# Kernel tuning notes

Measured on AMD Instinct MI355X. Metric: run time of the kernel, lower is better.

The kernel has to match this reference:

```python
import jax, jax.numpy as jnp
import numpy as np

N_NODES = 20000
N_EDGES = 640000
D = 128


def setup_inputs() -> dict:
    key = jax.random.key(0)
    ks = jax.random.split(key, 8)
    scale = 1.0 / np.sqrt(D)
    x = jax.random.normal(ks[0], (N_NODES, D), dtype=jnp.float32)
    edge_index = jax.random.randint(ks[1], (2, N_EDGES), 0, N_NODES, dtype=jnp.int64)
    W1_rel = jax.random.normal(ks[2], (D, D), dtype=jnp.float32) * scale
    b1_rel = jnp.zeros((D,), dtype=jnp.float32)
    W1_root = jax.random.normal(ks[3], (D, D), dtype=jnp.float32) * scale
    W2_rel = jax.random.normal(ks[4], (D, D), dtype=jnp.float32) * scale
    b2_rel = jnp.zeros((D,), dtype=jnp.float32)
    W2_root = jax.random.normal(ks[5], (D, D), dtype=jnp.float32) * scale
    return {"x": x, "edge_index": edge_index,
            "W1_rel": W1_rel, "b1_rel": b1_rel, "W1_root": W1_root,
            "W2_rel": W2_rel, "b2_rel": b2_rel, "W2_root": W2_root}


def _graph_conv(x, src, dst, W_rel, b_rel, W_root):
    # sum-aggregate neighbor features: gather from src, scatter-add to dst
    agg = jax.ops.segment_sum(x[src], dst, num_segments=N_NODES)  # [N, D]
    # PyG GraphConv: lin_rel(agg) (with bias) + lin_root(x) (no bias)
    return agg @ W_rel + b_rel + x @ W_root


def reference(x, edge_index, W1_rel, b1_rel, W1_root, W2_rel, b2_rel, W2_root):
    src, dst = edge_index[0], edge_index[1]  # messages flow src (j) -> dst (i)
    h = jax.nn.relu(_graph_conv(x, src, dst, W1_rel, b1_rel, W1_root))
    out = _graph_conv(h, src, dst, W2_rel, b2_rel, W2_root)  # final ReLU stripped
    return out
```

## Files before the change

kernel.cpp:

```cpp
#include <hip/hip_runtime.h>

#define N_NODES 20000
#define N_EDGES 640000
#define D 128
#define CAP 128

typedef __attribute__((ext_vector_type(8))) short bf16x8;
typedef __attribute__((ext_vector_type(4))) float f32x4;

__device__ __forceinline__ short f2bf(float f) {
    union { float f; unsigned u; } un; un.f = f;
    unsigned r = un.u + 0x7fff + ((un.u >> 16) & 1);
    return (short)(r >> 16);
}
__device__ __forceinline__ float bflo(unsigned u) { return __uint_as_float(u << 16); }
__device__ __forceinline__ float bfhi(unsigned u) { return __uint_as_float(u & 0xffff0000u); }

__global__ __launch_bounds__(256) void prep_kernel(
    const float* __restrict__ x,
    const int* __restrict__ src, const int* __restrict__ dst,
    const float* __restrict__ W1_rel, const float* __restrict__ W1_root,
    const float* __restrict__ W2_rel, const float* __restrict__ W2_root,
    int* __restrict__ cnt, unsigned short* __restrict__ buckets,
    short* __restrict__ xb, short* __restrict__ wpk1, short* __restrict__ wpk2)
{
    const int b = blockIdx.x;
    const int tid = threadIdx.x;
    if (b < 2500) {
        int e = b * 256 + tid;
        int d = dst[e];
        int s = src[e];
        int p = atomicAdd(&cnt[d], 1);
        if (p < CAP) buckets[(d << 7) + p] = (unsigned short)s;
    } else if (b < 5000) {
        int i = (b - 2500) * 256 + tid;
        float4 v = ((const float4*)x)[i];
        ushort4 o;
        o.x = (unsigned short)f2bf(v.x);
        o.y = (unsigned short)f2bf(v.y);
        o.z = (unsigned short)f2bf(v.z);
        o.w = (unsigned short)f2bf(v.w);
        ((ushort4*)xb)[i] = o;
    } else {
        int pb  = b - 5000;
        int job = pb >> 4;
        int idx = (pb & 15) * 256 + tid;
        const float* Wrel  = job ? W2_rel  : W1_rel;
        const float* Wroot = job ? W2_root : W1_root;
        short* Wpk = job ? wpk2 : wpk1;
        int lane = idx & 63;
        int ct   = (idx >> 6) & 7;
        int t    = idx >> 9;
        const float* W = (t < 4) ? Wrel : Wroot;
        int k0  = (t & 3) * 32 + (lane >> 4) * 8;
        int col = ct * 16 + (lane & 15);
        bf16x8 pk;
#pragma unroll
        for (int j = 0; j < 8; j++)
            pk[j] = f2bf(W[(size_t)(k0 + j) * D + col]);
        ((bf16x8*)Wpk)[idx] = pk;
    }
}

template <bool RELU, bool OUT_BF16>
__global__ __launch_bounds__(512) void layer_kernel(
    const short* __restrict__ xin,
    const int* __restrict__ cnt,
    const unsigned short* __restrict__ buckets,
    const short* __restrict__ Wpk,
    const float* __restrict__ brel,
    void* __restrict__ outp)
{
    __shared__ short sAgg[16][136];

    const int tid  = threadIdx.x;
    const int row0 = blockIdx.x * 16;

    {
        const int hw   = tid >> 5;
        const int lane = tid & 31;
        const int node = row0 + hw;
        int n = cnt[node];
        n = (n > CAP) ? CAP : n;
        uint2 idxpk = *(const uint2*)(buckets + (node << 7) + lane * 4);

        float4 acc = make_float4(0.f, 0.f, 0.f, 0.f);
        int i = 0;
        for (; i + 8 <= n; i += 8) {
            int baseLane = i >> 2;
            uint2 u[8];
#pragma unroll
            for (int q = 0; q < 8; q++) {
                unsigned word = __shfl((q & 2) ? idxpk.y : idxpk.x,
                                       baseLane + (q >> 2), 32);
                unsigned sidx = (q & 1) ? (word >> 16) : (word & 0xffffu);
                u[q] = *(const uint2*)(xin + (size_t)sidx * D + lane * 4);
            }
#pragma unroll
            for (int q = 0; q < 8; q++) {
                acc.x += bflo(u[q].x); acc.y += bfhi(u[q].x);
                acc.z += bflo(u[q].y); acc.w += bfhi(u[q].y);
            }
        }
        for (; i < n; i++) {
            unsigned word = __shfl((i & 2) ? idxpk.y : idxpk.x, i >> 2, 32);
            unsigned sidx = (i & 1) ? (word >> 16) : (word & 0xffffu);
            uint2 u0 = *(const uint2*)(xin + (size_t)sidx * D + lane * 4);
            acc.x += bflo(u0.x); acc.y += bfhi(u0.x);
            acc.z += bflo(u0.y); acc.w += bfhi(u0.y);
        }
        ushort4 o;
        o.x = (unsigned short)f2bf(acc.x);
        o.y = (unsigned short)f2bf(acc.y);
        o.z = (unsigned short)f2bf(acc.z);
        o.w = (unsigned short)f2bf(acc.w);
        *(ushort4*)&sAgg[hw][lane * 4] = o;
    }
    __syncthreads();

    const int wave = tid >> 6;
    const int lane = tid & 63;
    const int quad = lane >> 4;
    const int l16  = lane & 15;

    f32x4 acc = (f32x4){0.f, 0.f, 0.f, 0.f};
    const short* arow_x = xin + (size_t)(row0 + l16) * D + quad * 8;
    const bf16x8* wb = (const bf16x8*)Wpk + lane;

#pragma unroll
    for (int t = 0; t < 8; t++) {
        bf16x8 a;
        if (t < 4)
            a = *(const bf16x8*)&sAgg[l16][(t & 3) * 32 + quad * 8];
        else
            a = *(const bf16x8*)(arow_x + (t & 3) * 32);
        bf16x8 bfr = wb[(t * 8 + wave) * 64];
        acc = __builtin_amdgcn_mfma_f32_16x16x32_bf16(a, bfr, acc, 0, 0, 0);
    }

    const int col  = wave * 16 + l16;
    const int orow = row0 + quad * 4;
    const float bias = brel[col];
#pragma unroll
    for (int r = 0; r < 4; r++) {
        float v = acc[r] + bias;
        if (RELU) v = fmaxf(v, 0.f);
        if (OUT_BF16)
            ((short*)outp)[(size_t)(orow + r) * D + col] = f2bf(v);
        else
            ((float*)outp)[(size_t)(orow + r) * D + col] = v;
    }
}

extern "C" void kernel_launch(void* const* d_in, const int* in_sizes, int n_in,
                              void* d_out, int out_size, void* d_ws, size_t ws_size,
                              hipStream_t stream) {
    const float* x       = (const float*)d_in[0];
    const int*   ei      = (const int*)  d_in[1];
    const float* W1_rel  = (const float*)d_in[2];
    const float* b1_rel  = (const float*)d_in[3];
    const float* W1_root = (const float*)d_in[4];
    const float* W2_rel  = (const float*)d_in[5];
    const float* b2_rel  = (const float*)d_in[6];
    const float* W2_root = (const float*)d_in[7];
    float* out = (float*)d_out;

    char* p = (char*)d_ws;
    short* xb   = (short*)p;  p += (size_t)N_NODES * D * 2;
    short* hb   = (short*)p;  p += (size_t)N_NODES * D * 2;
    short* wpk1 = (short*)p;  p += 65536;
    short* wpk2 = (short*)p;  p += 65536;
    int*   cnt  = (int*)p;    p += (size_t)N_NODES * 4;
    unsigned short* buckets = (unsigned short*)p;

    const int* src = ei;
    const int* dst = ei + N_EDGES;

    const int layerblocks = N_NODES / 16;

    hipMemsetAsync(cnt, 0, (size_t)N_NODES * sizeof(int), stream);
    prep_kernel<<<5032, 256, 0, stream>>>(
        x, src, dst, W1_rel, W1_root, W2_rel, W2_root,
        cnt, buckets, xb, wpk1, wpk2);

    layer_kernel<true, true><<<layerblocks, 512, 0, stream>>>(
        xb, cnt, buckets, wpk1, b1_rel, (void*)hb);

    layer_kernel<false, false><<<layerblocks, 512, 0, stream>>>(
        hb, cnt, buckets, wpk2, b2_rel, (void*)out);
}
```

Baseline: 162.6 us.

## Replace global per-node atomic bucketing with two-pass binned CSR build

New measurement: 149.9 us. 1.08x faster.

```diff
diff --git a/kernel.cpp b/kernel.cpp
--- a/kernel.cpp
+++ b/kernel.cpp
@@ -4,6 +4,8 @@
 #define N_EDGES 640000
 #define D 128
 #define CAP 128
+#define NBINS 157
+#define BINCAP 4608
 
 typedef __attribute__((ext_vector_type(8))) short bf16x8;
 typedef __attribute__((ext_vector_type(4))) float f32x4;
@@ -21,19 +23,46 @@
     const int* __restrict__ src, const int* __restrict__ dst,
     const float* __restrict__ W1_rel, const float* __restrict__ W1_root,
     const float* __restrict__ W2_rel, const float* __restrict__ W2_root,
-    int* __restrict__ cnt, unsigned short* __restrict__ buckets,
+    int* __restrict__ binCursor, unsigned* __restrict__ binned,
     short* __restrict__ xb, short* __restrict__ wpk1, short* __restrict__ wpk2)
 {
     const int b = blockIdx.x;
     const int tid = threadIdx.x;
-    if (b < 2500) {
-        int e = b * 256 + tid;
-        int d = dst[e];
-        int s = src[e];
-        int p = atomicAdd(&cnt[d], 1);
-        if (p < CAP) buckets[(d << 7) + p] = (unsigned short)s;
-    } else if (b < 5000) {
-        int i = (b - 2500) * 256 + tid;
+    if (b < 256) {
+        __shared__ int hist[NBINS];
+        __shared__ int sBase[NBINS];
+        __shared__ int sOff[NBINS];
+        for (int i = tid; i < NBINS; i += 256) { hist[i] = 0; sOff[i] = 0; }
+        __syncthreads();
+        const int e0 = b * 2500;
+        int d[10], s[10];
+#pragma unroll
+        for (int k = 0; k < 10; k++) {
+            int idx = k * 256 + tid;
+            if (idx < 2500) {
+                d[k] = dst[e0 + idx];
+                s[k] = src[e0 + idx];
+                atomicAdd(&hist[d[k] >> 7], 1);
+            } else {
+                d[k] = -1;
+            }
+        }
+        __syncthreads();
+        for (int i = tid; i < NBINS; i += 256)
+            sBase[i] = atomicAdd(&binCursor[i], hist[i]);
+        __syncthreads();
+#pragma unroll
+        for (int k = 0; k < 10; k++) {
+            if (d[k] >= 0) {
+                int bin = d[k] >> 7;
+                int off = sBase[bin] + atomicAdd(&sOff[bin], 1);
+                if (off < BINCAP)
+                    binned[bin * BINCAP + off] =
+                        ((unsigned)(d[k] & 127) << 16) | (unsigned)s[k];
+            }
+        }
+    } else if (b < 2756) {
+        int i = (b - 256) * 256 + tid;
         float4 v = ((const float4*)x)[i];
         ushort4 o;
         o.x = (unsigned short)f2bf(v.x);
@@ -42,7 +71,7 @@
         o.w = (unsigned short)f2bf(v.w);
         ((ushort4*)xb)[i] = o;
     } else {
-        int pb  = b - 5000;
+        int pb  = b - 2756;
         int job = pb >> 4;
         int idx = (pb & 15) * 256 + tid;
         const float* Wrel  = job ? W2_rel  : W1_rel;
@@ -62,6 +91,30 @@
     }
 }
 
+__global__ __launch_bounds__(256) void binplace_kernel(
+    const unsigned* __restrict__ binned, const int* __restrict__ binCursor,
+    unsigned short* __restrict__ buckets, int* __restrict__ cnt)
+{
+    __shared__ int lcnt[128];
+    const int bin = blockIdx.x;
+    const int tid = threadIdx.x;
+    if (tid < 128) lcnt[tid] = 0;
+    __syncthreads();
+    int n = binCursor[bin];
+    if (n > BINCAP) n = BINCAP;
+    const unsigned* rec = binned + bin * BINCAP;
+    for (int i = tid; i < n; i += 256) {
+        unsigned u = rec[i];
+        int nl = (int)(u >> 16);
+        int slot = atomicAdd(&lcnt[nl], 1);
+        if (slot < CAP)
+            buckets[(((bin << 7) | nl) << 7) + slot] = (unsigned short)(u & 0xffffu);
+    }
+    __syncthreads();
+    int node = (bin << 7) + tid;
+    if (tid < 128 && node < N_NODES) cnt[node] = lcnt[tid];
+}
+
 template <bool RELU, bool OUT_BF16>
 __global__ __launch_bounds__(512) void layer_kernel(
     const short* __restrict__ xin,
@@ -172,16 +225,22 @@
     short* wpk2 = (short*)p;  p += 65536;
     int*   cnt  = (int*)p;    p += (size_t)N_NODES * 4;
     unsigned short* buckets = (unsigned short*)p;
+    p += (size_t)N_NODES * CAP * 2;
+    unsigned* binned = (unsigned*)p;
+    p += (size_t)NBINS * BINCAP * 4;
+    int* binCursor = (int*)p;
 
     const int* src = ei;
     const int* dst = ei + N_EDGES;
 
     const int layerblocks = N_NODES / 16;
 
-    hipMemsetAsync(cnt, 0, (size_t)N_NODES * sizeof(int), stream);
-    prep_kernel<<<5032, 256, 0, stream>>>(
+    hipMemsetAsync(binCursor, 0, (size_t)NBINS * sizeof(int), stream);
+    prep_kernel<<<2788, 256, 0, stream>>>(
         x, src, dst, W1_rel, W1_root, W2_rel, W2_root,
-        cnt, buckets, xb, wpk1, wpk2);
+        binCursor, binned, xb, wpk1, wpk2);
+
+    binplace_kernel<<<NBINS, 256, 0, stream>>>(binned, binCursor, buckets, cnt);
 
     layer_kernel<true, true><<<layerblocks, 512, 0, stream>>>(
         xb, cnt, buckets, wpk1, b1_rel, (void*)hb);
```

## Replace global-atomic edge bucketing with two-pass shared-memory binning

Applied to the files above, without the earlier changes.

Result: faster. 151.4 us (-6.9%).

```diff
diff --git a/kernel.cpp b/kernel.cpp
--- a/kernel.cpp
+++ b/kernel.cpp
@@ -4,6 +4,10 @@
 #define N_EDGES 640000
 #define D 128
 #define CAP 128
+#define NBINS 157
+#define PA_BLOCKS 256
+#define EPB 2500
+#define SLABCAP 40
 
 typedef __attribute__((ext_vector_type(8))) short bf16x8;
 typedef __attribute__((ext_vector_type(4))) float f32x4;
@@ -21,19 +25,32 @@
     const int* __restrict__ src, const int* __restrict__ dst,
     const float* __restrict__ W1_rel, const float* __restrict__ W1_root,
     const float* __restrict__ W2_rel, const float* __restrict__ W2_root,
-    int* __restrict__ cnt, unsigned short* __restrict__ buckets,
+    unsigned* __restrict__ binned, int* __restrict__ cnts,
     short* __restrict__ xb, short* __restrict__ wpk1, short* __restrict__ wpk2)
 {
     const int b = blockIdx.x;
     const int tid = threadIdx.x;
-    if (b < 2500) {
-        int e = b * 256 + tid;
-        int d = dst[e];
-        int s = src[e];
-        int p = atomicAdd(&cnt[d], 1);
-        if (p < CAP) buckets[(d << 7) + p] = (unsigned short)s;
-    } else if (b < 5000) {
-        int i = (b - 2500) * 256 + tid;
+    if (b < PA_BLOCKS) {
+        __shared__ int sOff[NBINS];
+        for (int i = tid; i < NBINS; i += 256) sOff[i] = 0;
+        __syncthreads();
+        const int e0 = b * EPB;
+        for (int idx = tid; idx < EPB; idx += 256) {
+            int d = dst[e0 + idx];
+            int s = src[e0 + idx];
+            int bin = d >> 7;
+            int off = atomicAdd(&sOff[bin], 1);
+            if (off < SLABCAP)
+                binned[(size_t)(bin * PA_BLOCKS + b) * SLABCAP + off] =
+                    ((unsigned)(d & 127) << 16) | (unsigned)s;
+        }
+        __syncthreads();
+        for (int i = tid; i < NBINS; i += 256) {
+            int c = sOff[i];
+            cnts[i * PA_BLOCKS + b] = (c > SLABCAP) ? SLABCAP : c;
+        }
+    } else if (b < PA_BLOCKS + 2500) {
+        int i = (b - PA_BLOCKS) * 256 + tid;
         float4 v = ((const float4*)x)[i];
         ushort4 o;
         o.x = (unsigned short)f2bf(v.x);
@@ -42,7 +59,7 @@
         o.w = (unsigned short)f2bf(v.w);
         ((ushort4*)xb)[i] = o;
     } else {
-        int pb  = b - 5000;
+        int pb  = b - (PA_BLOCKS + 2500);
         int job = pb >> 4;
         int idx = (pb & 15) * 256 + tid;
         const float* Wrel  = job ? W2_rel  : W1_rel;
@@ -62,6 +79,32 @@
     }
 }
 
+__global__ __launch_bounds__(256) void binplace_kernel(
+    const unsigned* __restrict__ binned, const int* __restrict__ cnts,
+    unsigned short* __restrict__ buckets, int* __restrict__ cnt)
+{
+    __shared__ int lcnt[128];
+    const int bin = blockIdx.x;
+    const int tid = threadIdx.x;
+    if (tid < 128) lcnt[tid] = 0;
+    __syncthreads();
+    int c = cnts[bin * PA_BLOCKS + tid];
+    const unsigned* rec = binned + (size_t)(bin * PA_BLOCKS + tid) * SLABCAP;
+    for (int i = 0; i < c; i++) {
+        unsigned u = rec[i];
+        int nl = (int)(u >> 16);
+        int slot = atomicAdd(&lcnt[nl], 1);
+        if (slot < CAP)
+            buckets[(((bin << 7) | nl) << 7) + slot] = (unsigned short)(u & 0xffffu);
+    }
+    __syncthreads();
+    int node = (bin << 7) + tid;
+    if (tid < 128 && node < N_NODES) {
+        int n = lcnt[tid];
+        cnt[node] = (n > CAP) ? CAP : n;
+    }
+}
+
 template <bool RELU, bool OUT_BF16>
 __global__ __launch_bounds__(512) void layer_kernel(
     const short* __restrict__ xin,
@@ -73,82 +116,99 @@
 {
     __shared__ short sAgg[16][136];
 
-    const int tid  = threadIdx.x;
-    const int row0 = blockIdx.x * 16;
-
-    {
-        const int hw   = tid >> 5;
-        const int lane = tid & 31;
-        const int node = row0 + hw;
-        int n = cnt[node];
-        n = (n > CAP) ? CAP : n;
-        uint2 idxpk = *(const uint2*)(buckets + (node << 7) + lane * 4);
-
-        float4 acc = make_float4(0.f, 0.f, 0.f, 0.f);
-        int i = 0;
-        for (; i + 8 <= n; i += 8) {
-            int baseLane = i >> 2;
-            uint2 u[8];
-#pragma unroll
-            for (int q = 0; q < 8; q++) {
-                unsigned word = __shfl((q & 2) ? idxpk.y : idxpk.x,
-                                       baseLane + (q >> 2), 32);
-                unsigned sidx = (q & 1) ? (word >> 16) : (word & 0xffffu);
-                u[q] = *(const uint2*)(xin + (size_t)sidx * D + lane * 4);
+    const int tid = threadIdx.x;
+
+    for (int half = 0; half < 2; half++) {
+        const int bin  = blockIdx.x * 2 + half;
+        const int row0 = bin * 16;
+        if (half) __syncthreads();
+
+        {
+            const int hw   = tid >> 5;
+            const int lane = tid & 31;
+            const int node = row0 + hw;
+            int n = cnt[node];
+            n = (n > CAP) ? CAP : n;
+            uint2 idxpk = *(const uint2*)(buckets + (node << 7) + lane * 4);
+
+            float4 acc = make_float4(0.f, 0.f, 0.f, 0.f);
+            int full8 = n & ~7;
+            int i = 0;
+            for (; i < full8; i += 8) {
+                int baseLane = i >> 2;
+                uint2 u[8];
+#pragma unroll
+                for (int q = 0; q < 8; q++) {
+                    unsigned word = __shfl((q & 2) ? idxpk.y : idxpk.x,
+                                           baseLane + (q >> 2), 32);
+                    unsigned sidx = (q & 1) ? (word >> 16) : (word & 0xffffu);
+                    u[q] = *(const uint2*)(xin + (size_t)sidx * D + lane * 4);
+                }
+#pragma unroll
+                for (int q = 0; q < 8; q++) {
+                    acc.x += bflo(u[q].x); acc.y += bfhi(u[q].x);
+                    acc.z += bflo(u[q].y); acc.w += bfhi(u[q].y);
+                }
             }
-#pragma unroll
-            for (int q = 0; q < 8; q++) {
-                acc.x += bflo(u[q].x); acc.y += bfhi(u[q].x);
-                acc.z += bflo(u[q].y); acc.w += bfhi(u[q].y);
+            if (i < n) {
+                uint2 u[8];
+#pragma unroll
+                for (int q = 0; q < 8; q++) {
+                    int j  = i + q;
+                    int jc = (j < n) ? j : (n - 1);
+                    unsigned word = __shfl((jc & 2) ? idxpk.y : idxpk.x,
+                                           jc >> 2, 32);
+                    unsigned sidx = (jc & 1) ? (word >> 16) : (word & 0xffffu);
+                    u[q] = *(const uint2*)(xin + (size_t)sidx * D + lane * 4);
+                }
+#pragma unroll
+                for (int q = 0; q < 8; q++) {
+                    float m = (i + q < n) ? 1.f : 0.f;
+                    acc.x += m * bflo(u[q].x); acc.y += m * bfhi(u[q].x);
+                    acc.z += m * bflo(u[q].y); acc.w += m * bfhi(u[q].y);
+                }
             }
-        }
-        for (; i < n; i++) {
-            unsigned word = __shfl((i & 2) ? idxpk.y : idxpk.x, i >> 2, 32);
-            unsigned sidx = (i & 1) ? (word >> 16) : (word & 0xffffu);
-            uint2 u0 = *(const uint2*)(xin + (size_t)sidx * D + lane * 4);
-            acc.x += bflo(u0.x); acc.y += bfhi(u0.x);
-            acc.z += bflo(u0.y); acc.w += bfhi(u0.y);
-        }
-        ushort4 o;
-        o.x = (unsigned short)f2bf(acc.x);
-        o.y = (unsigned short)f2bf(acc.y);
-        o.z = (unsigned short)f2bf(acc.z);
-        o.w = (unsigned short)f2bf(acc.w);
-        *(ushort4*)&sAgg[hw][lane * 4] = o;
-    }
-    __syncthreads();
-
-    const int wave = tid >> 6;
-    const int lane = tid & 63;
-    const int quad = lane >> 4;
-    const int l16  = lane & 15;
-
-    f32x4 acc = (f32x4){0.f, 0.f, 0.f, 0.f};
-    const short* arow_x = xin + (size_t)(row0 + l16) * D + quad * 8;
-    const bf16x8* wb = (const bf16x8*)Wpk + lane;
-
-#pragma unroll
-    for (int t = 0; t < 8; t++) {
-        bf16x8 a;
-        if (t < 4)
-            a = *(const bf16x8*)&sAgg[l16][(t & 3) * 32 + quad * 8];
-        else
-            a = *(const bf16x8*)(arow_x + (t & 3) * 32);
-        bf16x8 bfr = wb[(t * 8 + wave) * 64];
-        acc = __builtin_amdgcn_mfma_f32_16x16x32_bf16(a, bfr, acc, 0, 0, 0);
-    }
-
-    const int col  = wave * 16 + l16;
-    const int orow = row0 + quad * 4;
-    const float bias = brel[col];
-#pragma unroll
-    for (int r = 0; r < 4; r++) {
-        float v = acc[r] + bias;
-        if (RELU) v = fmaxf(v, 0.f);
-        if (OUT_BF16)
-            ((short*)outp)[(size_t)(orow + r) * D + col] = f2bf(v);
-        else
-            ((float*)outp)[(size_t)(orow + r) * D + col] = v;
+            ushort4 o;
+            o.x = (unsigned short)f2bf(acc.x);
+            o.y = (unsigned short)f2bf(acc.y);
+            o.z = (unsigned short)f2bf(acc.z);
+            o.w = (unsigned short)f2bf(acc.w);
+            *(ushort4*)&sAgg[hw][lane * 4] = o;
+        }
+        __syncthreads();
+
+        const int wave = tid >> 6;
+        const int lane = tid & 63;
+        const int quad = lane >> 4;
+        const int l16  = lane & 15;
+
+        f32x4 acc = (f32x4){0.f, 0.f, 0.f, 0.f};
+        const short* arow_x = xin + (size_t)(row0 + l16) * D + quad * 8;
+        const bf16x8* wb = (const bf16x8*)Wpk + lane;
+
+#pragma unroll
+        for (int t = 0; t < 8; t++) {
+            bf16x8 a;
+            if (t < 4)
+                a = *(const bf16x8*)&sAgg[l16][(t & 3) * 32 + quad * 8];
+            else
+                a = *(const bf16x8*)(arow_x + (t & 3) * 32);
+            bf16x8 bfr = wb[(t * 8 + wave) * 64];
+            acc = __builtin_amdgcn_mfma_f32_16x16x32_bf16(a, bfr, acc, 0, 0, 0);
+        }
+
+        const int col  = wave * 16 + l16;
+        const int orow = row0 + quad * 4;
+        const float bias = brel[col];
+#pragma unroll
+        for (int r = 0; r < 4; r++) {
+            float v = acc[r] + bias;
+            if (RELU) v = fmaxf(v, 0.f);
+            if (OUT_BF16)
+                ((short*)outp)[(size_t)(orow + r) * D + col] = f2bf(v);
+            else
+                ((float*)outp)[(size_t)(orow + r) * D + col] = v;
+        }
     }
 }
 
@@ -172,20 +232,23 @@
     short* wpk2 = (short*)p;  p += 65536;
     int*   cnt  = (int*)p;    p += (size_t)N_NODES * 4;
     unsigned short* buckets = (unsigned short*)p;
+    p += (size_t)NBINS * 128 * CAP * 2;
+    unsigned* binned = (unsigned*)p;
+    p += (size_t)NBINS * PA_BLOCKS * SLABCAP * 4;
+    int* cnts = (int*)p;
 
     const int* src = ei;
     const int* dst = ei + N_EDGES;
 
-    const int layerblocks = N_NODES / 16;
-
-    hipMemsetAsync(cnt, 0, (size_t)N_NODES * sizeof(int), stream);
-    prep_kernel<<<5032, 256, 0, stream>>>(
+    prep_kernel<<<PA_BLOCKS + 2500 + 32, 256, 0, stream>>>(
         x, src, dst, W1_rel, W1_root, W2_rel, W2_root,
-        cnt, buckets, xb, wpk1, wpk2);
-
-    layer_kernel<true, true><<<layerblocks, 512, 0, stream>>>(
+        binned, cnts, xb, wpk1, wpk2);
+
+    binplace_kernel<<<NBINS, 256, 0, stream>>>(binned, cnts, buckets, cnt);
+
+    layer_kernel<true, true><<<625, 512, 0, stream>>>(
         xb, cnt, buckets, wpk1, b1_rel, (void*)hb);
 
-    layer_kernel<false, false><<<layerblocks, 512, 0, stream>>>(
+    layer_kernel<false, false><<<625, 512, 0, stream>>>(
         hb, cnt, buckets, wpk2, b2_rel, (void*)out);
 }
```
